# Kernel optimization log

Hardware: AMD Instinct MI355X
Metric: run time of the kernel (lower is better)

## Reference

```python
import jax, jax.numpy as jnp
import numpy as np

D_MODEL = 1024
N_HEADS = 16
D_K = D_MODEL // N_HEADS
B, S = 4, 2048


def setup_inputs() -> dict:
    key = jax.random.key(0)
    ks = jax.random.split(key, 12)
    scale = 1.0 / np.sqrt(D_MODEL)
    inp = {
        "Q": jax.random.normal(ks[0], (B, S, D_MODEL), jnp.float32),
        "K": jax.random.normal(ks[1], (B, S, D_MODEL), jnp.float32),
        "V": jax.random.normal(ks[2], (B, S, D_MODEL), jnp.float32),
        # causal mask, broadcast over batch and heads; 0 -> masked
        "mask": jnp.tril(jnp.ones((S, S), jnp.int32))[None, None, :, :],
        "W_q": jax.random.normal(ks[3], (D_MODEL, D_MODEL), jnp.float32) * scale,
        "b_q": jnp.zeros((D_MODEL,), jnp.float32),
        "W_k": jax.random.normal(ks[4], (D_MODEL, D_MODEL), jnp.float32) * scale,
        "b_k": jnp.zeros((D_MODEL,), jnp.float32),
        "W_v": jax.random.normal(ks[5], (D_MODEL, D_MODEL), jnp.float32) * scale,
        "b_v": jnp.zeros((D_MODEL,), jnp.float32),
        "W_o": jax.random.normal(ks[6], (D_MODEL, D_MODEL), jnp.float32) * scale,
        "b_o": jnp.zeros((D_MODEL,), jnp.float32),
    }
    return inp


def _split_heads(x):
    b, s, _ = x.shape
    return x.reshape(b, s, N_HEADS, D_K).transpose(0, 2, 1, 3)  # [B,H,S,Dk]


def reference(Q, K, V, mask, W_q, b_q, W_k, b_k, W_v, b_v, W_o, b_o):
    # linear projections (torch Linear: x @ W.T + b)
    q = _split_heads(Q @ W_q.T + b_q)
    k = _split_heads(K @ W_k.T + b_k)
    v = _split_heads(V @ W_v.T + b_v)
    # scaled dot-product attention with manual softmax
    scores = jnp.einsum('bhqd,bhkd->bhqk', q, k) / jnp.sqrt(jnp.float32(D_K))
    scores = jnp.where(mask == 0, jnp.finfo(scores.dtype).min, scores)
    probs = jax.nn.softmax(scores, axis=-1)
    out = jnp.einsum('bhqk,bhkd->bhqd', probs, v)  # [B,H,S,Dk]
    out = out.transpose(0, 2, 1, 3).reshape(Q.shape[0], -1, D_MODEL)
    return out @ W_o.T + b_o
```

## Files before the change

kernel.cpp:

```cpp
#include <hip/hip_runtime.h>

#define DEV __device__ __forceinline__

typedef __attribute__((ext_vector_type(4))) float f32x4;
typedef __attribute__((ext_vector_type(4))) int i32x4;
typedef __attribute__((ext_vector_type(8))) short s16x8;
typedef __attribute__((ext_vector_type(8))) __bf16 bf16x8;

static constexpr int D_MODEL = 1024;
static constexpr int SEQ = 2048;
static constexpr int NB = 4;
static constexpr int NH = 16;

DEV unsigned short f2bf(float f) {
  unsigned int u = __builtin_bit_cast(unsigned int, f);
  u += 0x7fffu + ((u >> 16) & 1u);
  return (unsigned short)(u >> 16);
}

DEV s16x8 pack8(f32x4 a, f32x4 b) {
  s16x8 r;
  r[0] = (short)f2bf(a[0]); r[1] = (short)f2bf(a[1]);
  r[2] = (short)f2bf(a[2]); r[3] = (short)f2bf(a[3]);
  r[4] = (short)f2bf(b[0]); r[5] = (short)f2bf(b[1]);
  r[6] = (short)f2bf(b[2]); r[7] = (short)f2bf(b[3]);
  return r;
}

DEV f32x4 MFMA(s16x8 a, s16x8 b, f32x4 c) {
  return __builtin_amdgcn_mfma_f32_16x16x32_bf16(
      __builtin_bit_cast(bf16x8, a), __builtin_bit_cast(bf16x8, b), c, 0, 0, 0);
}

typedef const __attribute__((address_space(1))) void gas_t;
typedef __attribute__((address_space(3))) void las_t;
DEV void gload16(const void* g, void* l) {
  __builtin_amdgcn_global_load_lds((gas_t*)(unsigned long long)g,
                                   (las_t*)(unsigned int)(unsigned long long)l,
                                   16, 0, 0);
}

__global__ __launch_bounds__(256) void convert_all(
    const float* __restrict__ Q, const float* __restrict__ K,
    const float* __restrict__ V, const float* __restrict__ Wq,
    const float* __restrict__ Wk, const float* __restrict__ Wv,
    const float* __restrict__ Wo, unsigned short* __restrict__ ws) {
  constexpr int BIG = NB * SEQ * D_MODEL;
  constexpr int WN = D_MODEL * D_MODEL;
  constexpr int BIGB = BIG / 8 / 256;
  constexpr int WB = WN / 8 / 256;
  const int blk = blockIdx.x;
  const float* src;
  unsigned short* dst;
  int boff;
  if (blk < 3 * BIGB) {
    const int r = blk / BIGB;
    boff = blk - r * BIGB;
    src = (r == 0) ? Q : ((r == 1) ? K : V);
    dst = ws + (size_t)r * BIG;
  } else {
    const int r = (blk - 3 * BIGB) / WB;
    boff = (blk - 3 * BIGB) - r * WB;
    src = (r == 0) ? Wq : ((r == 1) ? Wk : ((r == 2) ? Wv : Wo));
    dst = ws + (size_t)3 * BIG + (size_t)r * WN;
  }
  const size_t idx = ((size_t)boff * 256 + threadIdx.x) * 8;
  f32x4 a = *(const f32x4*)(src + idx);
  f32x4 b = *(const f32x4*)(src + idx + 4);
  *(s16x8*)(dst + idx) = pack8(a, b);
}

template <int OUT_MODE>
__global__ __launch_bounds__(256) void gemm_bt(const unsigned short* __restrict__ Ap,
                                               const unsigned short* __restrict__ Wp,
                                               const float* __restrict__ bias,
                                               void* __restrict__ outp) {
  constexpr int K = 1024, BK = 64;
  __shared__ __align__(16) unsigned char ldsA[2][128 * BK * 2];
  __shared__ __align__(16) unsigned char ldsB[2][128 * BK * 2];

  const int tid = threadIdx.x;
  const int wid = tid >> 6, lane = tid & 63;
  const int g16 = lane >> 4, l16 = lane & 15;
  const int m0 = blockIdx.y * 128;
  const int n0 = blockIdx.x * 128;
  const int wm = (wid >> 1) * 64, wn = (wid & 1) * 64;

  f32x4 acc[4][4];
#pragma unroll
  for (int a = 0; a < 4; ++a)
#pragma unroll
    for (int b = 0; b < 4; ++b) acc[a][b] = f32x4{0.f, 0.f, 0.f, 0.f};

  auto stage = [&](int buf, int kt) {
    const int k0 = kt * BK;
#pragma unroll
    for (int t = 0; t < 4; ++t) {
      const int seg = wid * 4 + t;
      const int cid = seg * 64 + lane;
      const int r = cid >> 3;
      const int c = ((cid & 7) ^ (r & 7)) * 8;
      gload16(Ap + (size_t)(m0 + r) * K + k0 + c, ldsA[buf] + seg * 1024);
      gload16(Wp + (size_t)(n0 + r) * K + k0 + c, ldsB[buf] + seg * 1024);
    }
  };

  auto compute = [&](int buf) {
#pragma unroll
    for (int ks = 0; ks < 2; ++ks) {
      const int kb2 = (ks * 32 + g16 * 8) * 2;
      s16x8 af[4], bfr[4];
#pragma unroll
      for (int mf = 0; mf < 4; ++mf) {
        const int row = wm + mf * 16 + l16;
        af[mf] = *(const s16x8*)(ldsA[buf] + ((row * 128 + kb2) ^ ((row & 7) << 4)));
      }
#pragma unroll
      for (int nf = 0; nf < 4; ++nf) {
        const int row = wn + nf * 16 + l16;
        bfr[nf] = *(const s16x8*)(ldsB[buf] + ((row * 128 + kb2) ^ ((row & 7) << 4)));
      }
#pragma unroll
      for (int mf = 0; mf < 4; ++mf)
#pragma unroll
        for (int nf = 0; nf < 4; ++nf)
          acc[mf][nf] = MFMA(af[mf], bfr[nf], acc[mf][nf]);
    }
  };

  stage(0, 0);
  __syncthreads();
  int buf = 0;
#pragma unroll 1
  for (int kt = 0; kt < K / BK; ++kt) {
    if (kt + 1 < K / BK) stage(buf ^ 1, kt + 1);
    compute(buf);
    __syncthreads();
    buf ^= 1;
  }

#pragma unroll
  for (int nf = 0; nf < 4; ++nf) {
    const int n = n0 + wn + nf * 16 + l16;
    const float bv = bias[n];
#pragma unroll
    for (int mf = 0; mf < 4; ++mf) {
#pragma unroll
      for (int i = 0; i < 4; ++i) {
        const int m = m0 + wm + mf * 16 + g16 * 4 + i;
        float v = acc[mf][nf][i] + bv;
        if constexpr (OUT_MODE == 0 || OUT_MODE == 1) {
          if constexpr (OUT_MODE == 0) v *= 0.18033688011112042f;
          const int bh = (m >> 11) * NH + (n >> 6);
          ((unsigned short*)outp)[((size_t)bh * SEQ + (m & 2047)) * 64 + (n & 63)] =
              f2bf(v);
        } else if constexpr (OUT_MODE == 2) {
          const int bh = (m >> 11) * NH + (n >> 6);
          ((unsigned short*)outp)[((size_t)bh * 64 + (n & 63)) * SEQ + (m & 2047)] =
              f2bf(v);
        } else {
          ((float*)outp)[(size_t)m * D_MODEL + n] = v;
        }
      }
    }
  }
}

__global__ __launch_bounds__(256) void attn_kernel(
    const unsigned short* __restrict__ q, const unsigned short* __restrict__ k,
    const unsigned short* __restrict__ vT, unsigned short* __restrict__ ctx) {
  __shared__ __align__(16) unsigned char ldsK[2][64 * 64 * 2];
  __shared__ __align__(16) unsigned char ldsV[2][64 * 64 * 2];

  const int tid = threadIdx.x, wid = tid >> 6, lane = tid & 63;
  const int g16 = lane >> 4, l16 = lane & 15;
  const int bh = blockIdx.y;
  const int jj = blockIdx.x;
  const int tA = 31 - jj, tB = jj;
  const int qrA = tA * 64 + wid * 16, qrB = tB * 64 + wid * 16;
  const size_t qbase = (size_t)bh * SEQ;

  s16x8 qfA[2], qfB[2];
#pragma unroll
  for (int ks = 0; ks < 2; ++ks) {
    qfA[ks] = *(const s16x8*)(q + (qbase + qrA + l16) * 64 + ks * 32 + g16 * 8);
    qfB[ks] = *(const s16x8*)(q + (qbase + qrB + l16) * 64 + ks * 32 + g16 * 8);
  }

  float mA = -3.0e38f, lA = 0.f, mB = -3.0e38f, lB = 0.f;
  f32x4 oA[4], oB[4];
#pragma unroll
  for (int i = 0; i < 4; ++i) {
    oA[i] = f32x4{0.f, 0.f, 0.f, 0.f};
    oB[i] = f32x4{0.f, 0.f, 0.f, 0.f};
  }

  const int srcb = (lane & 48) + ((lane & 48) >> 2);
  const int srcA_lane = ((2 * g16) & 3) * 16 + l16;
  const int srcB_lane = ((2 * g16 + 1) & 3) * 16 + l16;
  const bool jsel = (g16 >> 1) != 0;

  auto stage = [&](int buf, int kt) {
    const int kv0 = kt * 64;
#pragma unroll
    for (int t = 0; t < 2; ++t) {
      const int seg = wid * 2 + t;
      const int cid = seg * 64 + lane;
      const int r = cid >> 3;
      const int c = ((cid & 7) ^ (r & 7)) * 8;
      gload16(k + (qbase + kv0 + r) * 64 + c, ldsK[buf] + seg * 1024);
      gload16(vT + ((size_t)bh * 64 + r) * SEQ + kv0 + c, ldsV[buf] + seg * 1024);
    }
  };

  auto softmax = [&](f32x4* sc, float& mrun, float& lrun, f32x4* o, bool diag,
                     s16x8* pa) {
    if (diag) {
#pragma unroll
      for (int jn = 0; jn < 4; ++jn)
#pragma unroll
        for (int i = 0; i < 4; ++i)
          if (jn * 16 + g16 * 4 + i > wid * 16 + l16) sc[jn][i] = -3.0e38f;
    }
    float tm = sc[0][0];
#pragma unroll
    for (int jn = 0; jn < 4; ++jn)
#pragma unroll
      for (int i = 0; i < 4; ++i) tm = fmaxf(tm, sc[jn][i]);
    tm = fmaxf(tm, __shfl_xor(tm, 16, 64));
    tm = fmaxf(tm, __shfl_xor(tm, 32, 64));
    const float mnew = fmaxf(mrun, tm);
    const float sca = exp2f(mrun - mnew);
    mrun = mnew;
    float tsum = 0.f;
    unsigned int pk[4][2];
#pragma unroll
    for (int jn = 0; jn < 4; ++jn) {
      const float p0 = exp2f(sc[jn][0] - mnew);
      const float p1 = exp2f(sc[jn][1] - mnew);
      const float p2 = exp2f(sc[jn][2] - mnew);
      const float p3 = exp2f(sc[jn][3] - mnew);
      tsum += (p0 + p1) + (p2 + p3);
      pk[jn][0] = (unsigned int)f2bf(p0) | ((unsigned int)f2bf(p1) << 16);
      pk[jn][1] = (unsigned int)f2bf(p2) | ((unsigned int)f2bf(p3) << 16);
    }
    tsum += __shfl_xor(tsum, 16, 64);
    tsum += __shfl_xor(tsum, 32, 64);
    lrun = lrun * sca + tsum;
#pragma unroll
    for (int i = 0; i < 4; ++i) {
      const float si = __shfl(sca, srcb + i, 64);
#pragma unroll
      for (int jd = 0; jd < 4; ++jd) o[jd][i] *= si;
    }
#pragma unroll
    for (int ks = 0; ks < 2; ++ks) {
      i32x4 w;
      int a0 = __shfl((int)pk[2 * ks][0], srcA_lane, 64);
      int a1 = __shfl((int)pk[2 * ks + 1][0], srcA_lane, 64);
      w[0] = jsel ? a1 : a0;
      int b0 = __shfl((int)pk[2 * ks][1], srcA_lane, 64);
      int b1 = __shfl((int)pk[2 * ks + 1][1], srcA_lane, 64);
      w[1] = jsel ? b1 : b0;
      int c0 = __shfl((int)pk[2 * ks][0], srcB_lane, 64);
      int c1 = __shfl((int)pk[2 * ks + 1][0], srcB_lane, 64);
      w[2] = jsel ? c1 : c0;
      int d0 = __shfl((int)pk[2 * ks][1], srcB_lane, 64);
      int d1 = __shfl((int)pk[2 * ks + 1][1], srcB_lane, 64);
      w[3] = jsel ? d1 : d0;
      pa[ks] = __builtin_bit_cast(s16x8, w);
    }
  };

  stage(0, 0);
  __syncthreads();
  int buf = 0;
#pragma unroll 1
  for (int kt = 0; kt <= tA; ++kt) {
    if (kt < tA) stage(buf ^ 1, kt + 1);
    const bool doB = (kt <= tB);
    f32x4 scA[4], scB[4];
#pragma unroll
    for (int jn = 0; jn < 4; ++jn) {
      scA[jn] = f32x4{0.f, 0.f, 0.f, 0.f};
      scB[jn] = f32x4{0.f, 0.f, 0.f, 0.f};
    }
#pragma unroll
    for (int ks = 0; ks < 2; ++ks) {
      const int kb2 = (ks * 32 + g16 * 8) * 2;
#pragma unroll
      for (int jn = 0; jn < 4; ++jn) {
        const int row = jn * 16 + l16;
        s16x8 kf = *(const s16x8*)(ldsK[buf] + ((row * 128 + kb2) ^ ((row & 7) << 4)));
        scA[jn] = MFMA(kf, qfA[ks], scA[jn]);
        if (doB) scB[jn] = MFMA(kf, qfB[ks], scB[jn]);
      }
    }
    s16x8 paA[2], paB[2];
    softmax(scA, mA, lA, oA, kt == tA, paA);
    if (doB) softmax(scB, mB, lB, oB, kt == tB, paB);
#pragma unroll
    for (int ks = 0; ks < 2; ++ks) {
      const int kb2 = (ks * 32 + g16 * 8) * 2;
#pragma unroll
      for (int jd = 0; jd < 4; ++jd) {
        const int row = jd * 16 + l16;
        s16x8 vf = *(const s16x8*)(ldsV[buf] + ((row * 128 + kb2) ^ ((row & 7) << 4)));
        oA[jd] = MFMA(paA[ks], vf, oA[jd]);
        if (doB) oB[jd] = MFMA(paB[ks], vf, oB[jd]);
      }
    }
    __syncthreads();
    buf ^= 1;
  }

  const int b = bh >> 4, h = bh & 15;
  auto epi = [&](const f32x4* o, float lrun, int qr) {
#pragma unroll
    for (int i = 0; i < 4; ++i) {
      const float li = 1.f / __shfl(lrun, srcb + i, 64);
      const int qi = qr + g16 * 4 + i;
      unsigned short* dst = ctx + ((size_t)(b * SEQ + qi)) * D_MODEL + h * 64;
#pragma unroll
      for (int jd = 0; jd < 4; ++jd) dst[jd * 16 + l16] = f2bf(o[jd][i] * li);
    }
  };
  epi(oA, lA, qrA);
  epi(oB, lB, qrB);
}

extern "C" void kernel_launch(void* const* d_in, const int* in_sizes, int n_in,
                              void* d_out, int out_size, void* d_ws, size_t ws_size,
                              hipStream_t stream) {
  const float* Q = (const float*)d_in[0];
  const float* Kin = (const float*)d_in[1];
  const float* V = (const float*)d_in[2];
  const float* Wq = (const float*)d_in[4];
  const float* bq = (const float*)d_in[5];
  const float* Wk = (const float*)d_in[6];
  const float* bk = (const float*)d_in[7];
  const float* Wv = (const float*)d_in[8];
  const float* bv = (const float*)d_in[9];
  const float* Wo = (const float*)d_in[10];
  const float* bo = (const float*)d_in[11];
  float* out = (float*)d_out;

  constexpr size_t BIG = (size_t)NB * SEQ * D_MODEL;
  constexpr size_t WN = (size_t)D_MODEL * D_MODEL;
  unsigned short* ws = (unsigned short*)d_ws;
  unsigned short* Qb = ws;
  unsigned short* Kb = ws + BIG;
  unsigned short* Vb = ws + 2 * BIG;
  unsigned short* Wqb = ws + 3 * BIG;
  unsigned short* Wkb = Wqb + WN;
  unsigned short* Wvb = Wkb + WN;
  unsigned short* Wob = Wvb + WN;
  unsigned short* qb = Wob + WN;
  unsigned short* kb = qb + BIG;
  unsigned short* vTb = kb + BIG;
  unsigned short* ctx = Qb;

  dim3 blk(256);
  convert_all<<<dim3(3 * 4096 + 4 * 512), blk, 0, stream>>>(Q, Kin, V, Wq, Wk, Wv,
                                                            Wo, ws);
  dim3 grid(D_MODEL / 128, NB * SEQ / 128);
  gemm_bt<0><<<grid, blk, 0, stream>>>(Qb, Wqb, bq, qb);
  gemm_bt<1><<<grid, blk, 0, stream>>>(Kb, Wkb, bk, kb);
  gemm_bt<2><<<grid, blk, 0, stream>>>(Vb, Wvb, bv, vTb);
  attn_kernel<<<dim3(16, NB * NH), blk, 0, stream>>>(qb, kb, vTb, ctx);
  gemm_bt<3><<<grid, blk, 0, stream>>>(ctx, Wob, bo, out);
}
```

Before: 407.8 us.

## Batch QKV GEMMs into one launch and rework attention softmax layout

Merges the three projection GEMMs into a single launch that uses blockIdx.z to pick Q, K or V. In the attention kernel, the K/V LDS swizzle and read offsets are remapped so the score accumulator layout feeds the PV MFMA directly, which removes the cross-lane shuffles that repacked P. The running max is now rescaled only when it grows by more than a threshold (lazy rescaling), and s_setprio is raised around the MFMA blocks. Bf16 conversion switches to native casts. The threshold trick leaves unnormalized exponentials that can grow up to 2^8, which adds some risk to precision.

```diff
diff --git a/kernel.cpp b/kernel.cpp
--- a/kernel.cpp
+++ b/kernel.cpp
@@ -3,7 +3,6 @@
 #define DEV __device__ __forceinline__
 
 typedef __attribute__((ext_vector_type(4))) float f32x4;
-typedef __attribute__((ext_vector_type(4))) int i32x4;
 typedef __attribute__((ext_vector_type(8))) short s16x8;
 typedef __attribute__((ext_vector_type(8))) __bf16 bf16x8;
 
@@ -13,18 +12,15 @@
 static constexpr int NH = 16;
 
 DEV unsigned short f2bf(float f) {
-  unsigned int u = __builtin_bit_cast(unsigned int, f);
-  u += 0x7fffu + ((u >> 16) & 1u);
-  return (unsigned short)(u >> 16);
+  __bf16 h = (__bf16)f;
+  return __builtin_bit_cast(unsigned short, h);
 }
 
 DEV s16x8 pack8(f32x4 a, f32x4 b) {
-  s16x8 r;
-  r[0] = (short)f2bf(a[0]); r[1] = (short)f2bf(a[1]);
-  r[2] = (short)f2bf(a[2]); r[3] = (short)f2bf(a[3]);
-  r[4] = (short)f2bf(b[0]); r[5] = (short)f2bf(b[1]);
-  r[6] = (short)f2bf(b[2]); r[7] = (short)f2bf(b[3]);
-  return r;
+  bf16x8 r;
+  r[0] = (__bf16)a[0]; r[1] = (__bf16)a[1]; r[2] = (__bf16)a[2]; r[3] = (__bf16)a[3];
+  r[4] = (__bf16)b[0]; r[5] = (__bf16)b[1]; r[6] = (__bf16)b[2]; r[7] = (__bf16)b[3];
+  return __builtin_bit_cast(s16x8, r);
 }
 
 DEV f32x4 MFMA(s16x8 a, s16x8 b, f32x4 c) {
@@ -70,14 +66,22 @@
   *(s16x8*)(dst + idx) = pack8(a, b);
 }
 
-template <int OUT_MODE>
-__global__ __launch_bounds__(256) void gemm_bt(const unsigned short* __restrict__ Ap,
-                                               const unsigned short* __restrict__ Wp,
-                                               const float* __restrict__ bias,
-                                               void* __restrict__ outp) {
+__global__ __launch_bounds__(256) void qkv_gemm(const unsigned short* __restrict__ ws,
+                                                const float* __restrict__ bq,
+                                                const float* __restrict__ bk,
+                                                const float* __restrict__ bv,
+                                                unsigned short* __restrict__ outb) {
   constexpr int K = 1024, BK = 64;
+  constexpr size_t BIG = (size_t)NB * SEQ * D_MODEL;
+  constexpr size_t WN = (size_t)D_MODEL * D_MODEL;
   __shared__ __align__(16) unsigned char ldsA[2][128 * BK * 2];
   __shared__ __align__(16) unsigned char ldsB[2][128 * BK * 2];
+
+  const int z = blockIdx.z;
+  const unsigned short* Ap = ws + (size_t)z * BIG;
+  const unsigned short* Wp = ws + 3 * BIG + (size_t)z * WN;
+  const float* bias = (z == 0) ? bq : ((z == 1) ? bk : bv);
+  unsigned short* outp = outb + (size_t)z * BIG;
 
   const int tid = threadIdx.x;
   const int wid = tid >> 6, lane = tid & 63;
@@ -142,25 +146,103 @@
 #pragma unroll
   for (int nf = 0; nf < 4; ++nf) {
     const int n = n0 + wn + nf * 16 + l16;
-    const float bv = bias[n];
+    const float bv_ = bias[n];
 #pragma unroll
     for (int mf = 0; mf < 4; ++mf) {
 #pragma unroll
       for (int i = 0; i < 4; ++i) {
         const int m = m0 + wm + mf * 16 + g16 * 4 + i;
-        float v = acc[mf][nf][i] + bv;
-        if constexpr (OUT_MODE == 0 || OUT_MODE == 1) {
-          if constexpr (OUT_MODE == 0) v *= 0.18033688011112042f;
-          const int bh = (m >> 11) * NH + (n >> 6);
-          ((unsigned short*)outp)[((size_t)bh * SEQ + (m & 2047)) * 64 + (n & 63)] =
-              f2bf(v);
-        } else if constexpr (OUT_MODE == 2) {
-          const int bh = (m >> 11) * NH + (n >> 6);
-          ((unsigned short*)outp)[((size_t)bh * 64 + (n & 63)) * SEQ + (m & 2047)] =
-              f2bf(v);
+        float v = acc[mf][nf][i] + bv_;
+        if (z == 0) v *= 0.18033688011112042f;
+        const int bh = (m >> 11) * NH + (n >> 6);
+        if (z < 2) {
+          outp[((size_t)bh * SEQ + (m & 2047)) * 64 + (n & 63)] = f2bf(v);
         } else {
-          ((float*)outp)[(size_t)m * D_MODEL + n] = v;
+          outp[((size_t)bh * 64 + (n & 63)) * SEQ + (m & 2047)] = f2bf(v);
         }
+      }
+    }
+  }
+}
+
+__global__ __launch_bounds__(256) void gemm_out(const unsigned short* __restrict__ Ap,
+                                                const unsigned short* __restrict__ Wp,
+                                                const float* __restrict__ bias,
+                                                float* __restrict__ outp) {
+  constexpr int K = 1024, BK = 64;
+  __shared__ __align__(16) unsigned char ldsA[2][128 * BK * 2];
+  __shared__ __align__(16) unsigned char ldsB[2][128 * BK * 2];
+
+  const int tid = threadIdx.x;
+  const int wid = tid >> 6, lane = tid & 63;
+  const int g16 = lane >> 4, l16 = lane & 15;
+  const int m0 = blockIdx.y * 128;
+  const int n0 = blockIdx.x * 128;
+  const int wm = (wid >> 1) * 64, wn = (wid & 1) * 64;
+
+  f32x4 acc[4][4];
+#pragma unroll
+  for (int a = 0; a < 4; ++a)
+#pragma unroll
+    for (int b = 0; b < 4; ++b) acc[a][b] = f32x4{0.f, 0.f, 0.f, 0.f};
+
+  auto stage = [&](int buf, int kt) {
+    const int k0 = kt * BK;
+#pragma unroll
+    for (int t = 0; t < 4; ++t) {
+      const int seg = wid * 4 + t;
+      const int cid = seg * 64 + lane;
+      const int r = cid >> 3;
+      const int c = ((cid & 7) ^ (r & 7)) * 8;
+      gload16(Ap + (size_t)(m0 + r) * K + k0 + c, ldsA[buf] + seg * 1024);
+      gload16(Wp + (size_t)(n0 + r) * K + k0 + c, ldsB[buf] + seg * 1024);
+    }
+  };
+
+  auto compute = [&](int buf) {
+#pragma unroll
+    for (int ks = 0; ks < 2; ++ks) {
+      const int kb2 = (ks * 32 + g16 * 8) * 2;
+      s16x8 af[4], bfr[4];
+#pragma unroll
+      for (int mf = 0; mf < 4; ++mf) {
+        const int row = wm + mf * 16 + l16;
+        af[mf] = *(const s16x8*)(ldsA[buf] + ((row * 128 + kb2) ^ ((row & 7) << 4)));
+      }
+#pragma unroll
+      for (int nf = 0; nf < 4; ++nf) {
+        const int row = wn + nf * 16 + l16;
+        bfr[nf] = *(const s16x8*)(ldsB[buf] + ((row * 128 + kb2) ^ ((row & 7) << 4)));
+      }
+#pragma unroll
+      for (int mf = 0; mf < 4; ++mf)
+#pragma unroll
+        for (int nf = 0; nf < 4; ++nf)
+          acc[mf][nf] = MFMA(af[mf], bfr[nf], acc[mf][nf]);
+    }
+  };
+
+  stage(0, 0);
+  __syncthreads();
+  int buf = 0;
+#pragma unroll 1
+  for (int kt = 0; kt < K / BK; ++kt) {
+    if (kt + 1 < K / BK) stage(buf ^ 1, kt + 1);
+    compute(buf);
+    __syncthreads();
+    buf ^= 1;
+  }
+
+#pragma unroll
+  for (int nf = 0; nf < 4; ++nf) {
+    const int n = n0 + wn + nf * 16 + l16;
+    const float bv_ = bias[n];
+#pragma unroll
+    for (int mf = 0; mf < 4; ++mf) {
+#pragma unroll
+      for (int i = 0; i < 4; ++i) {
+        const int m = m0 + wm + mf * 16 + g16 * 4 + i;
+        outp[(size_t)m * D_MODEL + n] = acc[mf][nf][i] + bv_;
       }
     }
   }
@@ -196,9 +278,11 @@
   }
 
   const int srcb = (lane & 48) + ((lane & 48) >> 2);
-  const int srcA_lane = ((2 * g16) & 3) * 16 + l16;
-  const int srcB_lane = ((2 * g16 + 1) & 3) * 16 + l16;
-  const bool jsel = (g16 >> 1) != 0;
+
+  const int kRowB = (8 * (l16 >> 2) + (l16 & 3)) * 128;
+  const int vRowB = l16 * 128;
+  const int xiV = ((l16 & 3) | ((l16 >> 3) << 2)) << 4;
+  const int xiK = (l16 & 7) << 4;
 
   auto stage = [&](int buf, int kt) {
     const int kv0 = kt * 64;
@@ -207,7 +291,8 @@
       const int seg = wid * 2 + t;
       const int cid = seg * 64 + lane;
       const int r = cid >> 3;
-      const int c = ((cid & 7) ^ (r & 7)) * 8;
+      const int xi = (r & 3) | (((r >> 3) & 1) << 2);
+      const int c = ((cid & 7) ^ xi) * 8;
       gload16(k + (qbase + kv0 + r) * 64 + c, ldsK[buf] + seg * 1024);
       gload16(vT + ((size_t)bh * 64 + r) * SEQ + kv0 + c, ldsV[buf] + seg * 1024);
     }
@@ -219,56 +304,48 @@
 #pragma unroll
       for (int jn = 0; jn < 4; ++jn)
 #pragma unroll
-        for (int i = 0; i < 4; ++i)
-          if (jn * 16 + g16 * 4 + i > wid * 16 + l16) sc[jn][i] = -3.0e38f;
-    }
-    float tm = sc[0][0];
-#pragma unroll
-    for (int jn = 0; jn < 4; ++jn)
-#pragma unroll
-      for (int i = 0; i < 4; ++i) tm = fmaxf(tm, sc[jn][i]);
-    tm = fmaxf(tm, __shfl_xor(tm, 16, 64));
-    tm = fmaxf(tm, __shfl_xor(tm, 32, 64));
-    const float mnew = fmaxf(mrun, tm);
-    const float sca = exp2f(mrun - mnew);
-    mrun = mnew;
+        for (int i = 0; i < 4; ++i) {
+          const int kvp = 32 * (jn & 1) + 8 * g16 + 4 * (jn >> 1) + i;
+          if (kvp > wid * 16 + l16) sc[jn][i] = -3.0e38f;
+        }
+    }
+    float pm = fmaxf(fmaxf(fmaxf(sc[0][0], sc[0][1]), fmaxf(sc[0][2], sc[0][3])),
+                     fmaxf(fmaxf(sc[1][0], sc[1][1]), fmaxf(sc[1][2], sc[1][3])));
+    pm = fmaxf(pm,
+               fmaxf(fmaxf(fmaxf(sc[2][0], sc[2][1]), fmaxf(sc[2][2], sc[2][3])),
+                     fmaxf(fmaxf(sc[3][0], sc[3][1]), fmaxf(sc[3][2], sc[3][3]))));
+    pm = fmaxf(pm, __shfl_xor(pm, 16, 64));
+    pm = fmaxf(pm, __shfl_xor(pm, 32, 64));
+    if (__any(pm > mrun + 8.0f)) {
+      const float mnew = fmaxf(mrun, pm);
+      const float sca = exp2f(mrun - mnew);
+      lrun *= sca;
+#pragma unroll
+      for (int i = 0; i < 4; ++i) {
+        const float si = __shfl(sca, srcb + i, 64);
+#pragma unroll
+        for (int jd = 0; jd < 4; ++jd) o[jd][i] *= si;
+      }
+      mrun = mnew;
+    }
     float tsum = 0.f;
-    unsigned int pk[4][2];
 #pragma unroll
     for (int jn = 0; jn < 4; ++jn) {
-      const float p0 = exp2f(sc[jn][0] - mnew);
-      const float p1 = exp2f(sc[jn][1] - mnew);
-      const float p2 = exp2f(sc[jn][2] - mnew);
-      const float p3 = exp2f(sc[jn][3] - mnew);
-      tsum += (p0 + p1) + (p2 + p3);
-      pk[jn][0] = (unsigned int)f2bf(p0) | ((unsigned int)f2bf(p1) << 16);
-      pk[jn][1] = (unsigned int)f2bf(p2) | ((unsigned int)f2bf(p3) << 16);
+#pragma unroll
+      for (int i = 0; i < 4; ++i) sc[jn][i] = exp2f(sc[jn][i] - mrun);
+      tsum += (sc[jn][0] + sc[jn][1]) + (sc[jn][2] + sc[jn][3]);
     }
     tsum += __shfl_xor(tsum, 16, 64);
     tsum += __shfl_xor(tsum, 32, 64);
-    lrun = lrun * sca + tsum;
-#pragma unroll
-    for (int i = 0; i < 4; ++i) {
-      const float si = __shfl(sca, srcb + i, 64);
-#pragma unroll
-      for (int jd = 0; jd < 4; ++jd) o[jd][i] *= si;
-    }
+    lrun += tsum;
 #pragma unroll
     for (int ks = 0; ks < 2; ++ks) {
-      i32x4 w;
-      int a0 = __shfl((int)pk[2 * ks][0], srcA_lane, 64);
-      int a1 = __shfl((int)pk[2 * ks + 1][0], srcA_lane, 64);
-      w[0] = jsel ? a1 : a0;
-      int b0 = __shfl((int)pk[2 * ks][1], srcA_lane, 64);
-      int b1 = __shfl((int)pk[2 * ks + 1][1], srcA_lane, 64);
-      w[1] = jsel ? b1 : b0;
-      int c0 = __shfl((int)pk[2 * ks][0], srcB_lane, 64);
-      int c1 = __shfl((int)pk[2 * ks + 1][0], srcB_lane, 64);
-      w[2] = jsel ? c1 : c0;
-      int d0 = __shfl((int)pk[2 * ks][1], srcB_lane, 64);
-      int d1 = __shfl((int)pk[2 * ks + 1][1], srcB_lane, 64);
-      w[3] = jsel ? d1 : d0;
-      pa[ks] = __builtin_bit_cast(s16x8, w);
+      bf16x8 t;
+      t[0] = (__bf16)sc[ks][0]; t[1] = (__bf16)sc[ks][1];
+      t[2] = (__bf16)sc[ks][2]; t[3] = (__bf16)sc[ks][3];
+      t[4] = (__bf16)sc[ks + 2][0]; t[5] = (__bf16)sc[ks + 2][1];
+      t[6] = (__bf16)sc[ks + 2][2]; t[7] = (__bf16)sc[ks + 2][3];
+      pa[ks] = __builtin_bit_cast(s16x8, t);
     }
   };
 
@@ -285,31 +362,35 @@
       scA[jn] = f32x4{0.f, 0.f, 0.f, 0.f};
       scB[jn] = f32x4{0.f, 0.f, 0.f, 0.f};
     }
+    __builtin_amdgcn_s_setprio(1);
 #pragma unroll
     for (int ks = 0; ks < 2; ++ks) {
-      const int kb2 = (ks * 32 + g16 * 8) * 2;
+      const int klane = (ldsK[buf] - ldsK[0]) ? 0 : 0;
+      const int kb = ((64 * ks + 16 * g16) ^ xiK) + kRowB;
 #pragma unroll
       for (int jn = 0; jn < 4; ++jn) {
-        const int row = jn * 16 + l16;
-        s16x8 kf = *(const s16x8*)(ldsK[buf] + ((row * 128 + kb2) ^ ((row & 7) << 4)));
+        const int off = kb + 4096 * (jn & 1) + 512 * (jn >> 1);
+        s16x8 kf = *(const s16x8*)(ldsK[buf] + off);
         scA[jn] = MFMA(kf, qfA[ks], scA[jn]);
         if (doB) scB[jn] = MFMA(kf, qfB[ks], scB[jn]);
       }
     }
+    __builtin_amdgcn_s_setprio(0);
     s16x8 paA[2], paB[2];
     softmax(scA, mA, lA, oA, kt == tA, paA);
     if (doB) softmax(scB, mB, lB, oB, kt == tB, paB);
+    __builtin_amdgcn_s_setprio(1);
 #pragma unroll
     for (int ks = 0; ks < 2; ++ks) {
-      const int kb2 = (ks * 32 + g16 * 8) * 2;
+      const int vb = ((64 * ks + 16 * g16) ^ xiV) + vRowB;
 #pragma unroll
       for (int jd = 0; jd < 4; ++jd) {
-        const int row = jd * 16 + l16;
-        s16x8 vf = *(const s16x8*)(ldsV[buf] + ((row * 128 + kb2) ^ ((row & 7) << 4)));
+        s16x8 vf = *(const s16x8*)(ldsV[buf] + vb + 2048 * jd);
         oA[jd] = MFMA(paA[ks], vf, oA[jd]);
         if (doB) oB[jd] = MFMA(paB[ks], vf, oB[jd]);
       }
     }
+    __builtin_amdgcn_s_setprio(0);
     __syncthreads();
     buf ^= 1;
   }
@@ -349,13 +430,9 @@
   constexpr size_t WN = (size_t)D_MODEL * D_MODEL;
   unsigned short* ws = (unsigned short*)d_ws;
   unsigned short* Qb = ws;
-  unsigned short* Kb = ws + BIG;
-  unsigned short* Vb = ws + 2 * BIG;
-  unsigned short* Wqb = ws + 3 * BIG;
-  unsigned short* Wkb = Wqb + WN;
-  unsigned short* Wvb = Wkb + WN;
-  unsigned short* Wob = Wvb + WN;
-  unsigned short* qb = Wob + WN;
+  unsigned short* Wob = ws + 3 * BIG + 3 * WN;
+  unsigned short* qkv = Wob + WN;
+  unsigned short* qb = qkv;
   unsigned short* kb = qb + BIG;
   unsigned short* vTb = kb + BIG;
   unsigned short* ctx = Qb;
@@ -363,10 +440,9 @@
   dim3 blk(256);
   convert_all<<<dim3(3 * 4096 + 4 * 512), blk, 0, stream>>>(Q, Kin, V, Wq, Wk, Wv,
                                                             Wo, ws);
-  dim3 grid(D_MODEL / 128, NB * SEQ / 128);
-  gemm_bt<0><<<grid, blk, 0, stream>>>(Qb, Wqb, bq, qb);
-  gemm_bt<1><<<grid, blk, 0, stream>>>(Kb, Wkb, bk, kb);
-  gemm_bt<2><<<grid, blk, 0, stream>>>(Vb, Wvb, bv, vTb);
+  qkv_gemm<<<dim3(D_MODEL / 128, NB * SEQ / 128, 3), blk, 0, stream>>>(ws, bq, bk,
+                                                                       bv, qkv);
   attn_kernel<<<dim3(16, NB * NH), blk, 0, stream>>>(qb, kb, vTb, ctx);
-  gemm_bt<3><<<grid, blk, 0, stream>>>(ctx, Wob, bo, out);
-}
+  gemm_out<<<dim3(D_MODEL / 128, NB * SEQ / 128), blk, 0, stream>>>(ctx, Wob, bo,
+                                                                    out);
+}
```

New measurement: 391.9 us. 3.9% less time.
